# Optimization experiments

Hardware: AMD Instinct MI355X
Metric: run time of the kernel (lower is better)

The kernel has to match this reference:

```python
import jax, jax.numpy as jnp
import numpy as np

B = 16384          # batch
F = 256            # num_features
H1, H2 = 32, 16    # hidden_units


def setup_inputs() -> dict:
    key = jax.random.key(0)
    ks = jax.random.split(key, 7)
    return {
        "x":  jax.random.normal(ks[0], (B, F), dtype=jnp.float32),
        "W1": jax.random.normal(ks[1], (F, 1, H1), dtype=jnp.float32) * 0.5,
        "b1": jax.random.normal(ks[2], (F, H1), dtype=jnp.float32) * 0.1,
        "W2": jax.random.normal(ks[3], (F, H1, H2), dtype=jnp.float32) * (1.0 / np.sqrt(H1)),
        "b2": jax.random.normal(ks[4], (F, H2), dtype=jnp.float32) * 0.1,
        "W3": jax.random.normal(ks[5], (F, H2, 1), dtype=jnp.float32) * (1.0 / np.sqrt(H2)),
        "b3": jax.random.normal(ks[6], (F, 1), dtype=jnp.float32) * 0.1,
    }


def reference(x, W1, b1, W2, b2, W3, b3):
    # Per-feature tiny MLP 1->H1->H2->1, batched over features as grouped GEMMs.
    # x: [B, F] (each feature is a scalar input to its own network)
    h1 = jax.nn.relu(jnp.einsum('bf,fh->bfh', x, W1[:, 0, :]) + b1)          # [B,F,H1]
    h2 = jax.nn.relu(jnp.einsum('bfh,fhk->bfk', h1, W2) + b2)                 # [B,F,H2]
    contrib = jnp.einsum('bfk,fk->bf', h2, W3[:, :, 0]) + b3[:, 0]           # [B,F]
    out = jnp.sum(contrib, axis=1, keepdims=True)                             # [B,1]
    return jax.nn.sigmoid(out)
```

## Files before the change

### kernel.cpp

```cpp
#include <hip/hip_runtime.h>
#include <math.h>

#define B_TOTAL 16384
#define F_TOTAL 256
#define H1 32
#define H2 16
#define FPB 32
#define RPB 128

typedef _Float16 f16;
typedef __attribute__((ext_vector_type(2))) _Float16 f16x2;
typedef __attribute__((ext_vector_type(8))) _Float16 f16x8;
typedef __attribute__((ext_vector_type(4))) float floatx4;

union F8 { uint4 u; f16x2 h2[4]; f16x8 h8; };

__global__ __launch_bounds__(64) void nam_pack(
    const float* __restrict__ W1, const float* __restrict__ b1,
    const float* __restrict__ W2, const float* __restrict__ b2,
    const float* __restrict__ W3,
    uint4* __restrict__ pkB,
    uint4* __restrict__ pkW,
    float2* __restrict__ pkE)
{
    const int f = blockIdx.x;
    const int lane = threadIdx.x;
    const int n = lane & 15, q = lane >> 4;

    F8 H, L;
    #pragma unroll
    for (int j = 0; j < 8; ++j) {
        float w = W2[(size_t)f * (H1 * H2) + (q * 8 + j) * H2 + n];
        f16 hi = (f16)w;
        H.h8[j] = hi;
        L.h8[j] = (f16)(w - (float)hi);
    }
    pkB[(size_t)f * 128 + lane] = H.u;
    pkB[(size_t)f * 128 + 64 + lane] = L.u;

    if (n == 0) {
        F8 A, Bb;
        #pragma unroll
        for (int j = 0; j < 8; ++j) {
            A.h8[j]  = (f16)W1[(size_t)f * H1 + q * 8 + j];
            Bb.h8[j] = (f16)b1[(size_t)f * H1 + q * 8 + j];
        }
        pkW[((size_t)f * 4 + q) * 2]     = A.u;
        pkW[((size_t)f * 4 + q) * 2 + 1] = Bb.u;
    }
    if (q == 0) {
        float2 e;
        e.x = b2[(size_t)f * H2 + n];
        e.y = W3[(size_t)f * H2 + n];
        pkE[(size_t)f * 16 + n] = e;
    }
}

__global__ __launch_bounds__(256, 4) void nam_main(
    const float* __restrict__ x,
    const float* __restrict__ b3,
    const uint4* __restrict__ pkB,
    const uint4* __restrict__ pkW,
    const float2* __restrict__ pkE,
    float* __restrict__ part)
{
    __shared__ float  xs[FPB][RPB];
    __shared__ uint4  w1b1s[FPB * 4 * 2];
    __shared__ float2 b2w3s[FPB * 16];
    __shared__ float  b3s[FPB];

    const int t = threadIdx.x;
    const int lane = t & 63;
    const int wave = t >> 6;
    const int n = lane & 15, q = lane >> 4;
    const int b0 = blockIdx.x * RPB;
    const int f0 = blockIdx.y * FPB;

    {
        int r = t >> 1, c0 = (t & 1) * 16;
        const float4* xrow = (const float4*)(x + (size_t)(b0 + r) * F_TOTAL + f0 + c0);
        #pragma unroll
        for (int i = 0; i < 4; ++i) {
            float4 v = xrow[i];
            xs[c0 + i * 4 + 0][r] = v.x; xs[c0 + i * 4 + 1][r] = v.y;
            xs[c0 + i * 4 + 2][r] = v.z; xs[c0 + i * 4 + 3][r] = v.w;
        }
    }
    w1b1s[t] = pkW[(size_t)f0 * 8 + t];
    ((uint4*)b2w3s)[t] = ((const uint4*)pkE)[(size_t)f0 * 8 + t];
    if (t < FPB) b3s[t] = b3[f0 + t];
    __syncthreads();

    const uint4* pB = pkB + (size_t)f0 * 128 + lane;
    uint4 bh[2], bl[2];
    bh[0] = pB[0];   bl[0] = pB[64];
    bh[1] = pB[128]; bl[1] = pB[192];

    floatx4 acc1 = {0.f, 0.f, 0.f, 0.f};
    floatx4 acc2 = {0.f, 0.f, 0.f, 0.f};
    const int rb = wave * 32;
    const f16x2 z2 = {(f16)0, (f16)0};

    #pragma unroll 2
    for (int fi = 0; fi < FPB; ++fi) {
        F8 Bh, Bl;
        Bh.u = bh[fi & 1];
        Bl.u = bl[fi & 1];
        int nf = (fi + 2 < FPB) ? fi + 2 : fi;
        bh[fi & 1] = pB[(size_t)nf * 128];
        bl[fi & 1] = pB[(size_t)nf * 128 + 64];

        const float xm1 = xs[fi][rb + n];
        const float xm2 = xs[fi][rb + 16 + n];
        F8 W, Bi;
        W.u  = w1b1s[(fi * 4 + q) * 2];
        Bi.u = w1b1s[(fi * 4 + q) * 2 + 1];

        const f16 xh1 = (f16)xm1;
        const f16 xh2 = (f16)xm2;
        const f16x2 x1 = {xh1, xh1};
        const f16x2 x2 = {xh2, xh2};

        F8 A1, A2;
        #pragma unroll
        for (int tt = 0; tt < 4; ++tt) {
            f16x2 h1 = x1 * W.h2[tt] + Bi.h2[tt];
            f16x2 h2 = x2 * W.h2[tt] + Bi.h2[tt];
            A1.h2[tt] = __builtin_elementwise_max(h1, z2);
            A2.h2[tt] = __builtin_elementwise_max(h2, z2);
        }

        floatx4 c1 = {0.f, 0.f, 0.f, 0.f};
        floatx4 c2 = {0.f, 0.f, 0.f, 0.f};
        c1 = __builtin_amdgcn_mfma_f32_16x16x32_f16(A1.h8, Bh.h8, c1, 0, 0, 0);
        c1 = __builtin_amdgcn_mfma_f32_16x16x32_f16(A1.h8, Bl.h8, c1, 0, 0, 0);
        c2 = __builtin_amdgcn_mfma_f32_16x16x32_f16(A2.h8, Bh.h8, c2, 0, 0, 0);
        c2 = __builtin_amdgcn_mfma_f32_16x16x32_f16(A2.h8, Bl.h8, c2, 0, 0, 0);

        const float2 bw = b2w3s[fi * 16 + n];
        #pragma unroll
        for (int r = 0; r < 4; ++r) {
            float u1 = c1[r] + bw.x; u1 = u1 > 0.f ? u1 : 0.f;
            acc1[r] = fmaf(u1, bw.y, acc1[r]);
            float u2 = c2[r] + bw.x; u2 = u2 > 0.f ? u2 : 0.f;
            acc2[r] = fmaf(u2, bw.y, acc2[r]);
        }
    }

    float accb3 = 0.f;
    #pragma unroll
    for (int i = 0; i < FPB; ++i) accb3 += b3s[i];

    #pragma unroll
    for (int r = 0; r < 4; ++r) {
        float v1 = acc1[r], v2 = acc2[r];
        v1 += __shfl_xor(v1, 1); v2 += __shfl_xor(v2, 1);
        v1 += __shfl_xor(v1, 2); v2 += __shfl_xor(v2, 2);
        v1 += __shfl_xor(v1, 4); v2 += __shfl_xor(v2, 4);
        v1 += __shfl_xor(v1, 8); v2 += __shfl_xor(v2, 8);
        acc1[r] = v1; acc2[r] = v2;
    }
    if (n == 0) {
        float* dst = part + (size_t)blockIdx.y * B_TOTAL + b0 + rb;
        float4 o1, o2;
        o1.x = acc1[0] + accb3; o1.y = acc1[1] + accb3;
        o1.z = acc1[2] + accb3; o1.w = acc1[3] + accb3;
        o2.x = acc2[0] + accb3; o2.y = acc2[1] + accb3;
        o2.z = acc2[2] + accb3; o2.w = acc2[3] + accb3;
        *(float4*)(dst + q * 4)      = o1;
        *(float4*)(dst + 16 + q * 4) = o2;
    }
}

__global__ __launch_bounds__(256) void nam_finish(
    const float* __restrict__ part, float* __restrict__ out)
{
    const int b = blockIdx.x * 256 + threadIdx.x;
    float s = 0.f;
    #pragma unroll
    for (int g = 0; g < 8; ++g) s += part[(size_t)g * B_TOTAL + b];
    out[b] = 1.0f / (1.0f + expf(-s));
}

extern "C" void kernel_launch(void* const* d_in, const int* in_sizes, int n_in,
                              void* d_out, int out_size, void* d_ws, size_t ws_size,
                              hipStream_t stream) {
    const float* x  = (const float*)d_in[0];
    const float* W1 = (const float*)d_in[1];
    const float* b1 = (const float*)d_in[2];
    const float* W2 = (const float*)d_in[3];
    const float* b2 = (const float*)d_in[4];
    const float* W3 = (const float*)d_in[5];
    const float* b3 = (const float*)d_in[6];
    float* out = (float*)d_out;

    char* ws = (char*)d_ws;
    uint4*  pkB   = (uint4*)ws;
    uint4*  pkW   = (uint4*)(ws + (512 << 10));
    float2* pkE   = (float2*)(ws + (544 << 10));
    float*  partp = (float*)(ws + (576 << 10));

    nam_pack<<<F_TOTAL, 64, 0, stream>>>(W1, b1, W2, b2, W3, pkB, pkW, pkE);

    dim3 grid(B_TOTAL / RPB, F_TOTAL / FPB);
    nam_main<<<grid, 256, 0, stream>>>(x, b3, pkB, pkW, pkE, partp);

    nam_finish<<<B_TOTAL / 256, 256, 0, stream>>>(partp, out);
}
```

Measured before the change: 91.80 us.

## Fuse finish reduction into main kernel via last-block atomic counter, pack epilogue

Removes the separate finish kernel: each row-chunk block increments an atomic counter, and the last feature-group block sums the partials and applies the sigmoid. The counter reset and the b3 group sums move into the pack kernel. x is converted to duplicated f16 pairs when written to shared memory, and the b2/W3 epilogue uses packed float2 math. This trades one kernel launch for threadfences, an atomic and an extra barrier in every block.

```diff
diff --git a/kernel.cpp b/kernel.cpp
--- a/kernel.cpp
+++ b/kernel.cpp
@@ -7,21 +7,26 @@
 #define H2 16
 #define FPB 32
 #define RPB 128
+#define NGRP (F_TOTAL / FPB)
+#define NCHUNK (B_TOTAL / RPB)
 
 typedef _Float16 f16;
 typedef __attribute__((ext_vector_type(2))) _Float16 f16x2;
 typedef __attribute__((ext_vector_type(8))) _Float16 f16x8;
 typedef __attribute__((ext_vector_type(4))) float floatx4;
+typedef __attribute__((ext_vector_type(2))) float floatx2;
 
 union F8 { uint4 u; f16x2 h2[4]; f16x8 h8; };
 
 __global__ __launch_bounds__(64) void nam_pack(
     const float* __restrict__ W1, const float* __restrict__ b1,
     const float* __restrict__ W2, const float* __restrict__ b2,
-    const float* __restrict__ W3,
+    const float* __restrict__ W3, const float* __restrict__ b3,
     uint4* __restrict__ pkB,
     uint4* __restrict__ pkW,
-    float2* __restrict__ pkE)
+    float4* __restrict__ pkE,
+    float* __restrict__ b3g,
+    int* __restrict__ cnt)
 {
     const int f = blockIdx.x;
     const int lane = threadIdx.x;
@@ -49,25 +54,34 @@
         pkW[((size_t)f * 4 + q) * 2 + 1] = Bb.u;
     }
     if (q == 0) {
-        float2 e;
-        e.x = b2[(size_t)f * H2 + n];
-        e.y = W3[(size_t)f * H2 + n];
+        float bb = b2[(size_t)f * H2 + n];
+        float ww = W3[(size_t)f * H2 + n];
+        float4 e; e.x = bb; e.y = bb; e.z = ww; e.w = ww;
         pkE[(size_t)f * 16 + n] = e;
     }
+    if (lane == 0 && (f & (FPB - 1)) == 0) {
+        float s = 0.f;
+        #pragma unroll
+        for (int i = 0; i < FPB; ++i) s += b3[f + i];
+        b3g[f / FPB] = s;
+    }
+    if (lane == 0 && f < NCHUNK) cnt[f] = 0;
 }
 
 __global__ __launch_bounds__(256, 4) void nam_main(
     const float* __restrict__ x,
-    const float* __restrict__ b3,
     const uint4* __restrict__ pkB,
     const uint4* __restrict__ pkW,
-    const float2* __restrict__ pkE,
-    float* __restrict__ part)
+    const float4* __restrict__ pkE,
+    const float* __restrict__ b3g,
+    float* __restrict__ part,
+    int* __restrict__ cnt,
+    float* __restrict__ out)
 {
-    __shared__ float  xs[FPB][RPB];
+    __shared__ f16x2  xs[FPB][RPB];
     __shared__ uint4  w1b1s[FPB * 4 * 2];
-    __shared__ float2 b2w3s[FPB * 16];
-    __shared__ float  b3s[FPB];
+    __shared__ float4 b2w3s[FPB * 16];
+    __shared__ int    elect;
 
     const int t = threadIdx.x;
     const int lane = t & 63;
@@ -82,13 +96,16 @@
         #pragma unroll
         for (int i = 0; i < 4; ++i) {
             float4 v = xrow[i];
-            xs[c0 + i * 4 + 0][r] = v.x; xs[c0 + i * 4 + 1][r] = v.y;
-            xs[c0 + i * 4 + 2][r] = v.z; xs[c0 + i * 4 + 3][r] = v.w;
+            f16 h0 = (f16)v.x, h1 = (f16)v.y, h2 = (f16)v.z, h3 = (f16)v.w;
+            xs[c0 + i * 4 + 0][r] = (f16x2){h0, h0};
+            xs[c0 + i * 4 + 1][r] = (f16x2){h1, h1};
+            xs[c0 + i * 4 + 2][r] = (f16x2){h2, h2};
+            xs[c0 + i * 4 + 3][r] = (f16x2){h3, h3};
         }
     }
     w1b1s[t] = pkW[(size_t)f0 * 8 + t];
-    ((uint4*)b2w3s)[t] = ((const uint4*)pkE)[(size_t)f0 * 8 + t];
-    if (t < FPB) b3s[t] = b3[f0 + t];
+    ((uint4*)b2w3s)[t]       = ((const uint4*)pkE)[(size_t)f0 * 16 + t];
+    ((uint4*)b2w3s)[t + 256] = ((const uint4*)pkE)[(size_t)f0 * 16 + t + 256];
     __syncthreads();
 
     const uint4* pB = pkB + (size_t)f0 * 128 + lane;
@@ -96,8 +113,10 @@
     bh[0] = pB[0];   bl[0] = pB[64];
     bh[1] = pB[128]; bl[1] = pB[192];
 
-    floatx4 acc1 = {0.f, 0.f, 0.f, 0.f};
-    floatx4 acc2 = {0.f, 0.f, 0.f, 0.f};
+    floatx2 acc1a = {0.f, 0.f}, acc1b = {0.f, 0.f};
+    floatx2 acc2a = {0.f, 0.f}, acc2b = {0.f, 0.f};
+    const floatx4 zero4 = {0.f, 0.f, 0.f, 0.f};
+    const floatx2 zero2 = {0.f, 0.f};
     const int rb = wave * 32;
     const f16x2 z2 = {(f16)0, (f16)0};
 
@@ -110,16 +129,11 @@
         bh[fi & 1] = pB[(size_t)nf * 128];
         bl[fi & 1] = pB[(size_t)nf * 128 + 64];
 
-        const float xm1 = xs[fi][rb + n];
-        const float xm2 = xs[fi][rb + 16 + n];
+        const f16x2 x1 = xs[fi][rb + n];
+        const f16x2 x2 = xs[fi][rb + 16 + n];
         F8 W, Bi;
         W.u  = w1b1s[(fi * 4 + q) * 2];
         Bi.u = w1b1s[(fi * 4 + q) * 2 + 1];
-
-        const f16 xh1 = (f16)xm1;
-        const f16 xh2 = (f16)xm2;
-        const f16x2 x1 = {xh1, xh1};
-        const f16x2 x2 = {xh2, xh2};
 
         F8 A1, A2;
         #pragma unroll
@@ -130,27 +144,33 @@
             A2.h2[tt] = __builtin_elementwise_max(h2, z2);
         }
 
-        floatx4 c1 = {0.f, 0.f, 0.f, 0.f};
-        floatx4 c2 = {0.f, 0.f, 0.f, 0.f};
-        c1 = __builtin_amdgcn_mfma_f32_16x16x32_f16(A1.h8, Bh.h8, c1, 0, 0, 0);
+        floatx4 c1 = __builtin_amdgcn_mfma_f32_16x16x32_f16(A1.h8, Bh.h8, zero4, 0, 0, 0);
         c1 = __builtin_amdgcn_mfma_f32_16x16x32_f16(A1.h8, Bl.h8, c1, 0, 0, 0);
-        c2 = __builtin_amdgcn_mfma_f32_16x16x32_f16(A2.h8, Bh.h8, c2, 0, 0, 0);
+        floatx4 c2 = __builtin_amdgcn_mfma_f32_16x16x32_f16(A2.h8, Bh.h8, zero4, 0, 0, 0);
         c2 = __builtin_amdgcn_mfma_f32_16x16x32_f16(A2.h8, Bl.h8, c2, 0, 0, 0);
 
-        const float2 bw = b2w3s[fi * 16 + n];
-        #pragma unroll
-        for (int r = 0; r < 4; ++r) {
-            float u1 = c1[r] + bw.x; u1 = u1 > 0.f ? u1 : 0.f;
-            acc1[r] = fmaf(u1, bw.y, acc1[r]);
-            float u2 = c2[r] + bw.x; u2 = u2 > 0.f ? u2 : 0.f;
-            acc2[r] = fmaf(u2, bw.y, acc2[r]);
-        }
-    }
-
-    float accb3 = 0.f;
-    #pragma unroll
-    for (int i = 0; i < FPB; ++i) accb3 += b3s[i];
-
+        const float4 bw = b2w3s[fi * 16 + n];
+        const floatx2 bx = {bw.x, bw.y};
+        const floatx2 by = {bw.z, bw.w};
+        floatx2 u;
+        u = (floatx2){c1[0], c1[1]} + bx;
+        u = __builtin_elementwise_max(u, zero2);
+        acc1a = __builtin_elementwise_fma(u, by, acc1a);
+        u = (floatx2){c1[2], c1[3]} + bx;
+        u = __builtin_elementwise_max(u, zero2);
+        acc1b = __builtin_elementwise_fma(u, by, acc1b);
+        u = (floatx2){c2[0], c2[1]} + bx;
+        u = __builtin_elementwise_max(u, zero2);
+        acc2a = __builtin_elementwise_fma(u, by, acc2a);
+        u = (floatx2){c2[2], c2[3]} + bx;
+        u = __builtin_elementwise_max(u, zero2);
+        acc2b = __builtin_elementwise_fma(u, by, acc2b);
+    }
+
+    const float accb3 = b3g[blockIdx.y];
+
+    floatx4 acc1 = {acc1a.x, acc1a.y, acc1b.x, acc1b.y};
+    floatx4 acc2 = {acc2a.x, acc2a.y, acc2b.x, acc2b.y};
     #pragma unroll
     for (int r = 0; r < 4; ++r) {
         float v1 = acc1[r], v2 = acc2[r];
@@ -170,16 +190,21 @@
         *(float4*)(dst + q * 4)      = o1;
         *(float4*)(dst + 16 + q * 4) = o2;
     }
-}
-
-__global__ __launch_bounds__(256) void nam_finish(
-    const float* __restrict__ part, float* __restrict__ out)
-{
-    const int b = blockIdx.x * 256 + threadIdx.x;
-    float s = 0.f;
-    #pragma unroll
-    for (int g = 0; g < 8; ++g) s += part[(size_t)g * B_TOTAL + b];
-    out[b] = 1.0f / (1.0f + expf(-s));
+
+    __threadfence();
+    __syncthreads();
+    if (t == 0) elect = atomicAdd(&cnt[blockIdx.x], 1);
+    __syncthreads();
+    if (elect == NGRP - 1) {
+        __threadfence();
+        if (t < RPB) {
+            const int row = b0 + t;
+            float s = 0.f;
+            #pragma unroll
+            for (int g = 0; g < NGRP; ++g) s += part[(size_t)g * B_TOTAL + row];
+            out[row] = 1.0f / (1.0f + expf(-s));
+        }
+    }
 }
 
 extern "C" void kernel_launch(void* const* d_in, const int* in_sizes, int n_in,
@@ -197,13 +222,13 @@
     char* ws = (char*)d_ws;
     uint4*  pkB   = (uint4*)ws;
     uint4*  pkW   = (uint4*)(ws + (512 << 10));
-    float2* pkE   = (float2*)(ws + (544 << 10));
-    float*  partp = (float*)(ws + (576 << 10));
-
-    nam_pack<<<F_TOTAL, 64, 0, stream>>>(W1, b1, W2, b2, W3, pkB, pkW, pkE);
-
-    dim3 grid(B_TOTAL / RPB, F_TOTAL / FPB);
-    nam_main<<<grid, 256, 0, stream>>>(x, b3, pkB, pkW, pkE, partp);
-
-    nam_finish<<<B_TOTAL / 256, 256, 0, stream>>>(partp, out);
+    float4* pkE   = (float4*)(ws + (544 << 10));
+    float*  b3g   = (float*)(ws + (608 << 10));
+    int*    cnt   = (int*)(ws + (609 << 10));
+    float*  partp = (float*)(ws + (640 << 10));
+
+    nam_pack<<<F_TOTAL, 64, 0, stream>>>(W1, b1, W2, b2, W3, b3, pkB, pkW, pkE, b3g, cnt);
+
+    dim3 grid(NCHUNK, NGRP);
+    nam_main<<<grid, 256, 0, stream>>>(x, pkB, pkW, pkE, b3g, partp, cnt, out);
 }
```

Result: slower. 162.3 us (+76.8%).
